# Kernel tuning notes

Measured on AMD Instinct MI355X. Metric: run time of the kernel, lower is better.

The kernel has to match this reference:

```python
import jax, jax.numpy as jnp
import numpy as np


def setup_inputs() -> dict:
    key = jax.random.key(0)
    ks = jax.random.split(key, 8)
    B, N, D, E, S = 8, 4096, 1024, 64, 2
    H = D
    T = E * S  # total slots = 128
    return {
        "x": jax.random.normal(ks[0], (B, N, D), jnp.float32),
        "phi_w": jax.random.normal(ks[1], (T, D), jnp.float32) * 0.02,
        "fc1_w": jax.random.normal(ks[2], (E, H, D), jnp.float32) * 0.02,
        "fc1_b": jax.random.normal(ks[3], (E, H), jnp.float32) * 0.02,
        "fc2_w": jax.random.normal(ks[4], (E, D, H), jnp.float32) * 0.02,
        "fc2_b": jax.random.normal(ks[5], (E, D), jnp.float32) * 0.02,
        "out_w": jax.random.normal(ks[6], (D, D), jnp.float32) * 0.02,
        "out_b": jax.random.normal(ks[7], (D,), jnp.float32) * 0.02,
    }


def reference(x, phi_w, fc1_w, fc1_b, fc2_w, fc2_b, out_w, out_b):
    B, N, D = x.shape
    E, H, _ = fc1_w.shape
    T = phi_w.shape[0]
    S = T // E
    # dispatch logits: (B, N, T)
    logits = jnp.einsum('bnd,td->bnt', x, phi_w)
    dispatch_w = jax.nn.softmax(logits, axis=1)  # softmax over tokens
    combine_w = jax.nn.softmax(logits, axis=2)   # softmax over slots
    # dispatch: compress tokens -> slots, (B, T, D) -> (B, E, S, D)
    slots = jnp.einsum('bnt,bnd->btd', dispatch_w, x).reshape(B, E, S, D)
    # per-expert tiny MLP (no weight duplication over B)
    h = jnp.einsum('besd,ehd->besh', slots, fc1_w) + fc1_b[None, :, None, :]
    h = jax.nn.gelu(h, approximate=True)  # tanh approximation, matches torch
    out = jnp.einsum('besh,edh->besd', h, fc2_w) + fc2_b[None, :, None, :]
    out = out.reshape(B, T, D)
    # combine: expand slots -> tokens
    combined = jnp.einsum('bnt,btd->bnd', combine_w, out)
    output = jnp.einsum('bnd,od->bno', combined, out_w) + out_b
    aux_loss = jnp.asarray(0.0, dtype=x.dtype)
    return output, aux_loss
```

## Files before the change

### kernel.cpp

```cpp
#include <hip/hip_runtime.h>
#include <math.h>

#define B_ 8
#define N_ 4096
#define D_ 1024
#define E_ 64
#define T_ 128

using bf16   = __bf16;
using bf16x4 = __attribute__((ext_vector_type(4))) __bf16;
using bf16x8 = __attribute__((ext_vector_type(8))) __bf16;
using f32x4  = __attribute__((ext_vector_type(4))) float;

#define MFMA16(a, b, c) __builtin_amdgcn_mfma_f32_16x16x32_bf16(a, b, c, 0, 0, 0)
#define LDK 72

__device__ __forceinline__ bf16x8 ldsfrag(const bf16* p) {
  const int lane = threadIdx.x & 63;
  return *(const bf16x8*)(p + (lane & 15) * LDK + (lane >> 4) * 8);
}

__global__ void k_convert(const float* __restrict__ phi, const float* __restrict__ ow,
                          bf16* __restrict__ phi_bf, bf16* __restrict__ ow_bf)
{
  if (blockIdx.x < 128) {
    int i = blockIdx.x * 256 + threadIdx.x;
    float4 v = ((const float4*)phi)[i];
    ((bf16x4*)phi_bf)[i] = (bf16x4){(bf16)v.x, (bf16)v.y, (bf16)v.z, (bf16)v.w};
  } else {
    int i = (blockIdx.x - 128) * 256 + threadIdx.x;
    float4 v = ((const float4*)ow)[i];
    ((bf16x4*)ow_bf)[i] = (bf16x4){(bf16)v.x, (bf16)v.y, (bf16)v.z, (bf16)v.w};
  }
}

__global__ __launch_bounds__(256) void k_logits(
    const float* __restrict__ X, const bf16* __restrict__ Phi,
    float* __restrict__ L, bf16* __restrict__ Xbf)
{
  __shared__ bf16 As[64][LDK];
  __shared__ bf16 Bs[128][LDK];
  const int m0 = blockIdx.x * 64;
  const int tid = threadIdx.x;
  const int wave = tid >> 6, lane = tid & 63;
  const int wm = (wave >> 1) * 32;
  const int wn = (wave & 1) * 64;

  f32x4 acc[2][4];
#pragma unroll
  for (int i = 0; i < 2; ++i)
#pragma unroll
    for (int j = 0; j < 4; ++j) acc[i][j] = (f32x4){0.f, 0.f, 0.f, 0.f};

  const int ar = tid >> 2, ac = (tid & 3) * 16;
  const int br = tid >> 1, bc = (tid & 1) * 32;

  for (int k0 = 0; k0 < 1024; k0 += 64) {
    const float* xp = X + (long)(m0 + ar) * 1024 + k0 + ac;
    float4 v0 = *(const float4*)(xp + 0);
    float4 v1 = *(const float4*)(xp + 4);
    float4 v2 = *(const float4*)(xp + 8);
    float4 v3 = *(const float4*)(xp + 12);
    bf16x8 p0 = {(bf16)v0.x, (bf16)v0.y, (bf16)v0.z, (bf16)v0.w,
                 (bf16)v1.x, (bf16)v1.y, (bf16)v1.z, (bf16)v1.w};
    bf16x8 p1 = {(bf16)v2.x, (bf16)v2.y, (bf16)v2.z, (bf16)v2.w,
                 (bf16)v3.x, (bf16)v3.y, (bf16)v3.z, (bf16)v3.w};
    *(bf16x8*)&As[ar][ac]     = p0;
    *(bf16x8*)&As[ar][ac + 8] = p1;
    bf16* xo = Xbf + (long)(m0 + ar) * 1024 + k0 + ac;
    *(bf16x8*)xo       = p0;
    *(bf16x8*)(xo + 8) = p1;

    const bf16* pp = Phi + (long)br * 1024 + k0 + bc;
    *(bf16x8*)&Bs[br][bc + 0]  = *(const bf16x8*)(pp + 0);
    *(bf16x8*)&Bs[br][bc + 8]  = *(const bf16x8*)(pp + 8);
    *(bf16x8*)&Bs[br][bc + 16] = *(const bf16x8*)(pp + 16);
    *(bf16x8*)&Bs[br][bc + 24] = *(const bf16x8*)(pp + 24);
    __syncthreads();
#pragma unroll
    for (int kk = 0; kk < 64; kk += 32) {
      bf16x8 a0 = ldsfrag(&As[wm][kk]);
      bf16x8 a1 = ldsfrag(&As[wm + 16][kk]);
#pragma unroll
      for (int n = 0; n < 4; ++n) {
        bf16x8 bb = ldsfrag(&Bs[wn + n * 16][kk]);
        acc[0][n] = MFMA16(a0, bb, acc[0][n]);
        acc[1][n] = MFMA16(a1, bb, acc[1][n]);
      }
    }
    __syncthreads();
  }
  const int cc = lane & 15, rr = (lane >> 4) * 4;
#pragma unroll
  for (int m = 0; m < 2; ++m)
#pragma unroll
    for (int n = 0; n < 4; ++n)
#pragma unroll
      for (int j = 0; j < 4; ++j)
        L[(long)(m0 + wm + m * 16 + rr + j) * 128 + wn + n * 16 + cc] = acc[m][n][j];
}

__global__ __launch_bounds__(256) void disp_partial(const float* __restrict__ L,
    float* __restrict__ redM, float* __restrict__ redS)
{
  const int chunk = blockIdx.x;
  const int b     = blockIdx.y;
  const int t    = threadIdx.x & 127;
  const int half = threadIdx.x >> 7;
  const float* Lb = L + (long)b * N_ * T_;
  float m = -1e30f, s = 0.f;
  for (int i = 0; i < 64; ++i) {
    int n = chunk * 128 + i * 2 + half;
    float v = Lb[(long)n * T_ + t];
    if (v > m) { s = s * expf(m - v) + 1.f; m = v; }
    else       { s += expf(v - m); }
  }
  __shared__ float sm[128], ss[128];
  if (half) { sm[t] = m; ss[t] = s; }
  __syncthreads();
  if (!half) {
    float m2 = sm[t], s2 = ss[t];
    float nm = fmaxf(m, m2);
    float ns = s * expf(m - nm) + s2 * expf(m2 - nm);
    redM[((long)b * 32 + chunk) * 128 + t] = nm;
    redS[((long)b * 32 + chunk) * 128 + t] = ns;
  }
}

__global__ void disp_final(const float* __restrict__ redM, const float* __restrict__ redS,
                           float* __restrict__ Mf, float* __restrict__ Zf)
{
  int idx = blockIdx.x * 256 + threadIdx.x;
  int b = idx >> 7, t = idx & 127;
  float m = -1e30f, s = 0.f;
  for (int c = 0; c < 32; ++c) {
    float mc = redM[((long)b * 32 + c) * 128 + t];
    float sc = redS[((long)b * 32 + c) * 128 + t];
    float nm = fmaxf(m, mc);
    s = s * expf(m - nm) + sc * expf(mc - nm);
    m = nm;
  }
  Mf[idx] = m;
  Zf[idx] = 1.f / s;
}

__global__ __launch_bounds__(256) void k_dwt(const float* __restrict__ L,
    const float* __restrict__ Mf, const float* __restrict__ Zf, bf16* __restrict__ DWT)
{
  __shared__ float S[64][132];
  const int b = blockIdx.y, n0 = blockIdx.x * 64;
  const int tid = threadIdx.x;
  const int r = tid >> 2;
  const int c0 = (tid & 3) * 32;
  const float* Lp = L + ((long)b * N_ + n0 + r) * T_ + c0;
#pragma unroll
  for (int i = 0; i < 32; i += 4) {
    float4 v = *(const float4*)(Lp + i);
    int tb = b * 128 + c0 + i;
    S[r][c0 + i + 0] = expf(v.x - Mf[tb + 0]) * Zf[tb + 0];
    S[r][c0 + i + 1] = expf(v.y - Mf[tb + 1]) * Zf[tb + 1];
    S[r][c0 + i + 2] = expf(v.z - Mf[tb + 2]) * Zf[tb + 2];
    S[r][c0 + i + 3] = expf(v.w - Mf[tb + 3]) * Zf[tb + 3];
  }
  __syncthreads();
  const int nc = (tid & 7) * 8;
  for (int ti = tid >> 3; ti < 128; ti += 32) {
    bf16x8 o;
#pragma unroll
    for (int j = 0; j < 8; ++j) o[j] = (bf16)S[nc + j][ti];
    *(bf16x8*)(DWT + ((long)b * 128 + ti) * 4096 + n0 + nc) = o;
  }
}

__global__ __launch_bounds__(256) void k_cw(const float* __restrict__ L, bf16* __restrict__ CW)
{
  const int row  = blockIdx.x * 4 + (threadIdx.x >> 6);
  const int lane = threadIdx.x & 63;
  const float* Lr = L + (long)row * T_;
  float v0 = Lr[lane], v1 = Lr[lane + 64];
  float m = fmaxf(v0, v1);
#pragma unroll
  for (int o = 32; o; o >>= 1) m = fmaxf(m, __shfl_xor(m, o));
  float e0 = expf(v0 - m), e1 = expf(v1 - m);
  float s = e0 + e1;
#pragma unroll
  for (int o = 32; o; o >>= 1) s += __shfl_xor(s, o);
  float inv = 1.f / s;
  CW[(long)row * T_ + lane]      = (bf16)(e0 * inv);
  CW[(long)row * T_ + lane + 64] = (bf16)(e1 * inv);
}

__global__ __launch_bounds__(256) void k_slots(
    const bf16* __restrict__ DWT, const bf16* __restrict__ Xbf, float* __restrict__ Part)
{
  __shared__ bf16 As[128][LDK];
  __shared__ bf16 Bs[128][LDK];
  const int b = blockIdx.z >> 3, chunk = blockIdx.z & 7;
  const int d0 = blockIdx.x * 128;
  const int tid = threadIdx.x, wave = tid >> 6, lane = tid & 63;
  const int wm = (wave >> 1) * 64, wn = (wave & 1) * 64;

  f32x4 acc[4][4];
#pragma unroll
  for (int i = 0; i < 4; ++i)
#pragma unroll
    for (int j = 0; j < 4; ++j) acc[i][j] = (f32x4){0.f, 0.f, 0.f, 0.f};

  const int at = tid >> 1, anc = (tid & 1) * 32;
  const int bn = tid >> 2, bdc = (tid & 3) * 32;
  const long dwt_b = (long)b * 128 * 4096;
  const long x_b   = (long)b * 4096 * 1024;

  for (int k0 = 0; k0 < 512; k0 += 64) {
    const int nbase = chunk * 512 + k0;
    const bf16* ap = DWT + dwt_b + (long)at * 4096 + nbase + anc;
    *(bf16x8*)&As[at][anc + 0]  = *(const bf16x8*)(ap + 0);
    *(bf16x8*)&As[at][anc + 8]  = *(const bf16x8*)(ap + 8);
    *(bf16x8*)&As[at][anc + 16] = *(const bf16x8*)(ap + 16);
    *(bf16x8*)&As[at][anc + 24] = *(const bf16x8*)(ap + 24);
    const bf16* xp = Xbf + x_b + (long)(nbase + bn) * 1024 + d0 + bdc;
    bf16x8 q0 = *(const bf16x8*)(xp + 0);
    bf16x8 q1 = *(const bf16x8*)(xp + 8);
    bf16x8 q2 = *(const bf16x8*)(xp + 16);
    bf16x8 q3 = *(const bf16x8*)(xp + 24);
#pragma unroll
    for (int i = 0; i < 8; ++i) {
      Bs[bdc + i][bn]      = q0[i];
      Bs[bdc + 8 + i][bn]  = q1[i];
      Bs[bdc + 16 + i][bn] = q2[i];
      Bs[bdc + 24 + i][bn] = q3[i];
    }
    __syncthreads();
#pragma unroll
    for (int kk = 0; kk < 64; kk += 32) {
      bf16x8 af[4], bfr[4];
#pragma unroll
      for (int m = 0; m < 4; ++m) af[m]  = ldsfrag(&As[wm + m * 16][kk]);
#pragma unroll
      for (int n = 0; n < 4; ++n) bfr[n] = ldsfrag(&Bs[wn + n * 16][kk]);
#pragma unroll
      for (int m = 0; m < 4; ++m)
#pragma unroll
        for (int n = 0; n < 4; ++n)
          acc[m][n] = MFMA16(af[m], bfr[n], acc[m][n]);
    }
    __syncthreads();
  }
  const int cc = lane & 15, rr = (lane >> 4) * 4;
  float* Cp = Part + (long)(chunk * 8 + b) * 128 * 1024;
#pragma unroll
  for (int m = 0; m < 4; ++m)
#pragma unroll
    for (int n = 0; n < 4; ++n)
#pragma unroll
      for (int j = 0; j < 4; ++j)
        Cp[(long)(wm + m * 16 + rr + j) * 1024 + d0 + wn + n * 16 + cc] = acc[m][n][j];
}

__global__ void k_reduce8(const float* __restrict__ P, bf16* __restrict__ O)
{
  long base = ((long)blockIdx.x * 256 + threadIdx.x) * 4;
  float4 s = *(const float4*)(P + base);
  for (int c = 1; c < 8; ++c) {
    float4 v = *(const float4*)(P + (long)c * 1048576 + base);
    s.x += v.x; s.y += v.y; s.z += v.z; s.w += v.w;
  }
  *(bf16x4*)(O + base) = (bf16x4){(bf16)s.x, (bf16)s.y, (bf16)s.z, (bf16)s.w};
}

template<int GELU, int INL>
__global__ __launch_bounds__(256) void k_expert(
    const bf16* __restrict__ Ab, const float* __restrict__ W,
    const float* __restrict__ bias, bf16* __restrict__ Out)
{
  __shared__ bf16 As[16][LDK];
  __shared__ bf16 Bs[64][LDK];
  const int e = blockIdx.y;
  const int h0 = blockIdx.x * 64;
  const int tid = threadIdx.x, wave = tid >> 6, lane = tid & 63;
  f32x4 acc = (f32x4){0.f, 0.f, 0.f, 0.f};

  const int hr = tid >> 2, kc = (tid & 3) * 16;

  for (int k0 = 0; k0 < 1024; k0 += 64) {
    if (tid < 128) {
      int r = tid >> 3, akc = (tid & 7) * 8;
      long row = (INL == 0) ? (long)((r >> 1) * 128 + e * 2 + (r & 1)) : (long)(e * 16 + r);
      *(bf16x8*)&As[r][akc] = *(const bf16x8*)(Ab + row * 1024 + k0 + akc);
    }
    const float* wp = W + ((long)e * 1024 + h0 + hr) * 1024 + k0 + kc;
    float4 w0 = *(const float4*)(wp + 0);
    float4 w1 = *(const float4*)(wp + 4);
    float4 w2 = *(const float4*)(wp + 8);
    float4 w3 = *(const float4*)(wp + 12);
    bf16x8 p0 = {(bf16)w0.x, (bf16)w0.y, (bf16)w0.z, (bf16)w0.w,
                 (bf16)w1.x, (bf16)w1.y, (bf16)w1.z, (bf16)w1.w};
    bf16x8 p1 = {(bf16)w2.x, (bf16)w2.y, (bf16)w2.z, (bf16)w2.w,
                 (bf16)w3.x, (bf16)w3.y, (bf16)w3.z, (bf16)w3.w};
    *(bf16x8*)&Bs[hr][kc]     = p0;
    *(bf16x8*)&Bs[hr][kc + 8] = p1;
    __syncthreads();
#pragma unroll
    for (int kk = 0; kk < 64; kk += 32) {
      bf16x8 a  = ldsfrag(&As[0][kk]);
      bf16x8 bb = ldsfrag(&Bs[wave * 16][kk]);
      acc = MFMA16(a, bb, acc);
    }
    __syncthreads();
  }
  const int cc = lane & 15, rr = (lane >> 4) * 4;
  const int h = h0 + wave * 16 + cc;
  const float bs = bias[e * 1024 + h];
#pragma unroll
  for (int j = 0; j < 4; ++j) {
    float v = acc[j] + bs;
    if (GELU) {
      float x3 = v * v * v;
      v = 0.5f * v * (1.f + tanhf(0.7978845608028654f * (v + 0.044715f * x3)));
    }
    int m = rr + j;
    long orow = (INL == 0) ? (long)(e * 16 + m) : (long)((m >> 1) * 128 + e * 2 + (m & 1));
    Out[orow * 1024 + h] = (bf16)v;
  }
}

__global__ __launch_bounds__(256) void k_proj(
    const bf16* __restrict__ OWbf, const bf16* __restrict__ OS, bf16* __restrict__ PT)
{
  __shared__ bf16 As[64][LDK];
  __shared__ bf16 Bs[64][LDK];
  const int o0 = blockIdx.y * 64, t0 = blockIdx.x * 64;
  const int tid = threadIdx.x, wave = tid >> 6, lane = tid & 63;
  const int wm = (wave >> 1) * 32, wn = (wave & 1) * 32;
  f32x4 acc[2][2];
#pragma unroll
  for (int i = 0; i < 2; ++i)
#pragma unroll
    for (int j = 0; j < 2; ++j) acc[i][j] = (f32x4){0.f, 0.f, 0.f, 0.f};

  const int r = tid >> 2, kc = (tid & 3) * 16;
  for (int k0 = 0; k0 < 1024; k0 += 64) {
    const bf16* apo = OWbf + (long)(o0 + r) * 1024 + k0 + kc;
    *(bf16x8*)&As[r][kc]     = *(const bf16x8*)(apo + 0);
    *(bf16x8*)&As[r][kc + 8] = *(const bf16x8*)(apo + 8);
    const bf16* bpo = OS + (long)(t0 + r) * 1024 + k0 + kc;
    *(bf16x8*)&Bs[r][kc]     = *(const bf16x8*)(bpo + 0);
    *(bf16x8*)&Bs[r][kc + 8] = *(const bf16x8*)(bpo + 8);
    __syncthreads();
#pragma unroll
    for (int kk = 0; kk < 64; kk += 32) {
      bf16x8 a0 = ldsfrag(&As[wm][kk]);
      bf16x8 a1 = ldsfrag(&As[wm + 16][kk]);
      bf16x8 b0 = ldsfrag(&Bs[wn][kk]);
      bf16x8 b1 = ldsfrag(&Bs[wn + 16][kk]);
      acc[0][0] = MFMA16(a0, b0, acc[0][0]);
      acc[0][1] = MFMA16(a0, b1, acc[0][1]);
      acc[1][0] = MFMA16(a1, b0, acc[1][0]);
      acc[1][1] = MFMA16(a1, b1, acc[1][1]);
    }
    __syncthreads();
  }
  const int cc = lane & 15, rr = (lane >> 4) * 4;
#pragma unroll
  for (int m = 0; m < 2; ++m)
#pragma unroll
    for (int n = 0; n < 2; ++n)
#pragma unroll
      for (int j = 0; j < 4; ++j)
        PT[(long)(o0 + wm + m * 16 + rr + j) * 1024 + t0 + wn + n * 16 + cc] =
            (bf16)acc[m][n][j];
}

__global__ __launch_bounds__(256) void k_combine(
    const bf16* __restrict__ CW, const bf16* __restrict__ PT,
    const float* __restrict__ ob, float* __restrict__ O)
{
  __shared__ bf16 As[128][LDK];
  __shared__ bf16 Bs[128][LDK];
  const int b = blockIdx.z, m0 = blockIdx.y * 128, o0 = blockIdx.x * 128;
  const int tid = threadIdx.x, wave = tid >> 6, lane = tid & 63;
  const int wm = (wave >> 1) * 64, wn = (wave & 1) * 64;

  f32x4 acc[4][4];
#pragma unroll
  for (int i = 0; i < 4; ++i)
#pragma unroll
    for (int j = 0; j < 4; ++j) acc[i][j] = (f32x4){0.f, 0.f, 0.f, 0.f};

  const int r = tid >> 1, tc = (tid & 1) * 32;
  for (int k0 = 0; k0 < 128; k0 += 64) {
    const bf16* ap = CW + ((long)b * N_ + m0 + r) * 128 + k0 + tc;
    *(bf16x8*)&As[r][tc + 0]  = *(const bf16x8*)(ap + 0);
    *(bf16x8*)&As[r][tc + 8]  = *(const bf16x8*)(ap + 8);
    *(bf16x8*)&As[r][tc + 16] = *(const bf16x8*)(ap + 16);
    *(bf16x8*)&As[r][tc + 24] = *(const bf16x8*)(ap + 24);
    const bf16* bp = PT + (long)(o0 + r) * 1024 + b * 128 + k0 + tc;
    *(bf16x8*)&Bs[r][tc + 0]  = *(const bf16x8*)(bp + 0);
    *(bf16x8*)&Bs[r][tc + 8]  = *(const bf16x8*)(bp + 8);
    *(bf16x8*)&Bs[r][tc + 16] = *(const bf16x8*)(bp + 16);
    *(bf16x8*)&Bs[r][tc + 24] = *(const bf16x8*)(bp + 24);
    __syncthreads();
#pragma unroll
    for (int kk = 0; kk < 64; kk += 32) {
      bf16x8 af[4], bfr[4];
#pragma unroll
      for (int m = 0; m < 4; ++m) af[m]  = ldsfrag(&As[wm + m * 16][kk]);
#pragma unroll
      for (int n = 0; n < 4; ++n) bfr[n] = ldsfrag(&Bs[wn + n * 16][kk]);
#pragma unroll
      for (int m = 0; m < 4; ++m)
#pragma unroll
        for (int n = 0; n < 4; ++n)
          acc[m][n] = MFMA16(af[m], bfr[n], acc[m][n]);
    }
    __syncthreads();
  }
  const int cc = lane & 15, rr = (lane >> 4) * 4;
#pragma unroll
  for (int n = 0; n < 4; ++n) {
    const int o = o0 + wn + n * 16 + cc;
    const float bv = ob[o];
#pragma unroll
    for (int m = 0; m < 4; ++m)
#pragma unroll
      for (int j = 0; j < 4; ++j)
        O[((long)b * N_ + m0 + wm + m * 16 + rr + j) * 1024 + o] = acc[m][n][j] + bv;
  }
}

__global__ void write_aux(float* __restrict__ out) { out[(long)B_ * N_ * D_] = 0.f; }

extern "C" void kernel_launch(void* const* d_in, const int* in_sizes, int n_in,
                              void* d_out, int out_size, void* d_ws, size_t ws_size,
                              hipStream_t stream)
{
  const float* x     = (const float*)d_in[0];
  const float* phi_w = (const float*)d_in[1];
  const float* fc1_w = (const float*)d_in[2];
  const float* fc1_b = (const float*)d_in[3];
  const float* fc2_w = (const float*)d_in[4];
  const float* fc2_b = (const float*)d_in[5];
  const float* out_w = (const float*)d_in[6];
  const float* out_b = (const float*)d_in[7];
  float* out = (float*)d_out;

  float* ws     = (float*)d_ws;
  float* logits = ws;
  float* redM   = logits + 4194304;
  float* redS   = redM + 32768;
  float* Mf     = redS + 32768;
  float* Zf     = Mf + 1024;
  bf16* DWT     = (bf16*)(Zf + 1024);
  bf16* CW      = DWT + 4194304;
  bf16* slots   = CW + 4194304;
  bf16* hbuf    = slots + 1048576;
  bf16* outs    = hbuf + 1048576;
  bf16* projT   = outs + 1048576;
  bf16* phi_bf  = projT + 1048576;
  bf16* outw_bf = phi_bf + 131072;

  bf16* Xbf   = (bf16*)d_out;
  float* Part = (float*)d_out + 16777216;

  k_convert<<<dim3(1152), 256, 0, stream>>>(phi_w, out_w, phi_bf, outw_bf);
  k_logits<<<dim3(512), 256, 0, stream>>>(x, phi_bf, logits, Xbf);
  disp_partial<<<dim3(32, 8), 256, 0, stream>>>(logits, redM, redS);
  disp_final<<<dim3(4), 256, 0, stream>>>(redM, redS, Mf, Zf);
  k_dwt<<<dim3(64, 8), 256, 0, stream>>>(logits, Mf, Zf, DWT);
  k_cw<<<dim3(8192), 256, 0, stream>>>(logits, CW);
  k_slots<<<dim3(8, 1, 64), 256, 0, stream>>>(DWT, Xbf, Part);
  k_reduce8<<<dim3(1024), 256, 0, stream>>>(Part, slots);
  k_expert<1, 0><<<dim3(16, 64), 256, 0, stream>>>(slots, fc1_w, fc1_b, hbuf);
  k_expert<0, 1><<<dim3(16, 64), 256, 0, stream>>>(hbuf, fc2_w, fc2_b, outs);
  k_proj<<<dim3(16, 16), 256, 0, stream>>>(outw_bf, outs, projT);
  k_combine<<<dim3(8, 32, 8), 256, 0, stream>>>(CW, projT, out_b, out);
  write_aux<<<1, 1, 0, stream>>>(out);
}
```

Before: 344.1 us.

## Fuse combine softmax and dispatch partial reductions into logits GEMM epilogue

The logits GEMM now stages its output tile in shared memory and computes the per-token combine softmax (writing CW) plus per-64-row online max/sum partials for the dispatch softmax. This removes the separate k_cw and disp_partial kernels and their re-reads of the logits buffer. disp_final now reduces twice as many chunks, k_dwt applies the exp/normalise during its transpose, and the aux-zero write moves into k_combine. The cost is extra epilogue work and a serial 64-row loop in the GEMM blocks that may lengthen their tail.

```diff
diff --git a/kernel.cpp b/kernel.cpp
--- a/kernel.cpp
+++ b/kernel.cpp
@@ -18,6 +18,11 @@
 __device__ __forceinline__ bf16x8 ldsfrag(const bf16* p) {
   const int lane = threadIdx.x & 63;
   return *(const bf16x8*)(p + (lane & 15) * LDK + (lane >> 4) * 8);
+}
+
+__device__ __forceinline__ bf16x8 cvt8(float4 a, float4 b) {
+  return (bf16x8){(bf16)a.x, (bf16)a.y, (bf16)a.z, (bf16)a.w,
+                  (bf16)b.x, (bf16)b.y, (bf16)b.z, (bf16)b.w};
 }
 
 __global__ void k_convert(const float* __restrict__ phi, const float* __restrict__ ow,
@@ -36,10 +41,14 @@
 
 __global__ __launch_bounds__(256) void k_logits(
     const float* __restrict__ X, const bf16* __restrict__ Phi,
-    float* __restrict__ L, bf16* __restrict__ Xbf)
-{
-  __shared__ bf16 As[64][LDK];
-  __shared__ bf16 Bs[128][LDK];
+    float* __restrict__ L, bf16* __restrict__ Xbf, bf16* __restrict__ CW,
+    float* __restrict__ redM, float* __restrict__ redS)
+{
+  __shared__ __align__(16) char smraw[34048];
+  bf16 (*As)[LDK] = (bf16(*)[LDK])smraw;
+  bf16 (*Bs)[LDK] = (bf16(*)[LDK])(smraw + 64 * LDK * 2);
+  float (*S)[133] = (float(*)[133])smraw;
+
   const int m0 = blockIdx.x * 64;
   const int tid = threadIdx.x;
   const int wave = tid >> 6, lane = tid & 63;
@@ -61,10 +70,8 @@
     float4 v1 = *(const float4*)(xp + 4);
     float4 v2 = *(const float4*)(xp + 8);
     float4 v3 = *(const float4*)(xp + 12);
-    bf16x8 p0 = {(bf16)v0.x, (bf16)v0.y, (bf16)v0.z, (bf16)v0.w,
-                 (bf16)v1.x, (bf16)v1.y, (bf16)v1.z, (bf16)v1.w};
-    bf16x8 p1 = {(bf16)v2.x, (bf16)v2.y, (bf16)v2.z, (bf16)v2.w,
-                 (bf16)v3.x, (bf16)v3.y, (bf16)v3.z, (bf16)v3.w};
+    bf16x8 p0 = cvt8(v0, v1);
+    bf16x8 p1 = cvt8(v2, v3);
     *(bf16x8*)&As[ar][ac]     = p0;
     *(bf16x8*)&As[ar][ac + 8] = p1;
     bf16* xo = Xbf + (long)(m0 + ar) * 1024 + k0 + ac;
@@ -96,34 +103,47 @@
 #pragma unroll
     for (int n = 0; n < 4; ++n)
 #pragma unroll
-      for (int j = 0; j < 4; ++j)
-        L[(long)(m0 + wm + m * 16 + rr + j) * 128 + wn + n * 16 + cc] = acc[m][n][j];
-}
-
-__global__ __launch_bounds__(256) void disp_partial(const float* __restrict__ L,
-    float* __restrict__ redM, float* __restrict__ redS)
-{
-  const int chunk = blockIdx.x;
-  const int b     = blockIdx.y;
-  const int t    = threadIdx.x & 127;
-  const int half = threadIdx.x >> 7;
-  const float* Lb = L + (long)b * N_ * T_;
-  float m = -1e30f, s = 0.f;
-  for (int i = 0; i < 64; ++i) {
-    int n = chunk * 128 + i * 2 + half;
-    float v = Lb[(long)n * T_ + t];
-    if (v > m) { s = s * expf(m - v) + 1.f; m = v; }
-    else       { s += expf(v - m); }
-  }
-  __shared__ float sm[128], ss[128];
-  if (half) { sm[t] = m; ss[t] = s; }
+      for (int j = 0; j < 4; ++j) {
+        const float val = acc[m][n][j];
+        L[(long)(m0 + wm + m * 16 + rr + j) * 128 + wn + n * 16 + cc] = val;
+        S[wm + m * 16 + rr + j][wn + n * 16 + cc] = val;
+      }
   __syncthreads();
-  if (!half) {
-    float m2 = sm[t], s2 = ss[t];
-    float nm = fmaxf(m, m2);
-    float ns = s * expf(m - nm) + s2 * expf(m2 - nm);
-    redM[((long)b * 32 + chunk) * 128 + t] = nm;
-    redS[((long)b * 32 + chunk) * 128 + t] = ns;
+
+  const int r = tid >> 2, q = tid & 3;
+  float v[32];
+#pragma unroll
+  for (int i = 0; i < 8; ++i)
+#pragma unroll
+    for (int j = 0; j < 4; ++j) v[i * 4 + j] = S[r][q * 4 + i * 16 + j];
+  float mx = -1e30f;
+#pragma unroll
+  for (int i = 0; i < 32; ++i) mx = fmaxf(mx, v[i]);
+  mx = fmaxf(mx, __shfl_xor(mx, 1));
+  mx = fmaxf(mx, __shfl_xor(mx, 2));
+  float sum = 0.f;
+#pragma unroll
+  for (int i = 0; i < 32; ++i) { v[i] = expf(v[i] - mx); sum += v[i]; }
+  sum += __shfl_xor(sum, 1);
+  sum += __shfl_xor(sum, 2);
+  const float inv = 1.f / sum;
+  bf16* cwr = CW + (long)(m0 + r) * 128 + q * 4;
+#pragma unroll
+  for (int i = 0; i < 8; ++i)
+    *(bf16x4*)(cwr + i * 16) = (bf16x4){(bf16)(v[i*4+0]*inv), (bf16)(v[i*4+1]*inv),
+                                        (bf16)(v[i*4+2]*inv), (bf16)(v[i*4+3]*inv)};
+
+  if (tid < 128) {
+    const int t = tid;
+    float m = -1e30f, s = 0.f;
+    for (int rj = 0; rj < 64; ++rj) {
+      float val = S[rj][t];
+      if (val > m) { s = s * expf(m - val) + 1.f; m = val; }
+      else         { s += expf(val - m); }
+    }
+    const long chunk = m0 >> 6;
+    redM[chunk * 128 + t] = m;
+    redS[chunk * 128 + t] = s;
   }
 }
 
@@ -133,9 +153,9 @@
   int idx = blockIdx.x * 256 + threadIdx.x;
   int b = idx >> 7, t = idx & 127;
   float m = -1e30f, s = 0.f;
-  for (int c = 0; c < 32; ++c) {
-    float mc = redM[((long)b * 32 + c) * 128 + t];
-    float sc = redS[((long)b * 32 + c) * 128 + t];
+  for (int c = 0; c < 64; ++c) {
+    float mc = redM[((long)b * 64 + c) * 128 + t];
+    float sc = redS[((long)b * 64 + c) * 128 + t];
     float nm = fmaxf(m, mc);
     s = s * expf(m - nm) + sc * expf(mc - nm);
     m = nm;
@@ -156,38 +176,20 @@
 #pragma unroll
   for (int i = 0; i < 32; i += 4) {
     float4 v = *(const float4*)(Lp + i);
-    int tb = b * 128 + c0 + i;
-    S[r][c0 + i + 0] = expf(v.x - Mf[tb + 0]) * Zf[tb + 0];
-    S[r][c0 + i + 1] = expf(v.y - Mf[tb + 1]) * Zf[tb + 1];
-    S[r][c0 + i + 2] = expf(v.z - Mf[tb + 2]) * Zf[tb + 2];
-    S[r][c0 + i + 3] = expf(v.w - Mf[tb + 3]) * Zf[tb + 3];
+    S[r][c0 + i + 0] = v.x;
+    S[r][c0 + i + 1] = v.y;
+    S[r][c0 + i + 2] = v.z;
+    S[r][c0 + i + 3] = v.w;
   }
   __syncthreads();
   const int nc = (tid & 7) * 8;
   for (int ti = tid >> 3; ti < 128; ti += 32) {
+    const float mf = Mf[b * 128 + ti], zf = Zf[b * 128 + ti];
     bf16x8 o;
 #pragma unroll
-    for (int j = 0; j < 8; ++j) o[j] = (bf16)S[nc + j][ti];
+    for (int j = 0; j < 8; ++j) o[j] = (bf16)(expf(S[nc + j][ti] - mf) * zf);
     *(bf16x8*)(DWT + ((long)b * 128 + ti) * 4096 + n0 + nc) = o;
   }
-}
-
-__global__ __launch_bounds__(256) void k_cw(const float* __restrict__ L, bf16* __restrict__ CW)
-{
-  const int row  = blockIdx.x * 4 + (threadIdx.x >> 6);
-  const int lane = threadIdx.x & 63;
-  const float* Lr = L + (long)row * T_;
-  float v0 = Lr[lane], v1 = Lr[lane + 64];
-  float m = fmaxf(v0, v1);
-#pragma unroll
-  for (int o = 32; o; o >>= 1) m = fmaxf(m, __shfl_xor(m, o));
-  float e0 = expf(v0 - m), e1 = expf(v1 - m);
-  float s = e0 + e1;
-#pragma unroll
-  for (int o = 32; o; o >>= 1) s += __shfl_xor(s, o);
-  float inv = 1.f / s;
-  CW[(long)row * T_ + lane]      = (bf16)(e0 * inv);
-  CW[(long)row * T_ + lane + 64] = (bf16)(e1 * inv);
 }
 
 __global__ __launch_bounds__(256) void k_slots(
@@ -247,7 +249,7 @@
     __syncthreads();
   }
   const int cc = lane & 15, rr = (lane >> 4) * 4;
-  float* Cp = Part + (long)(chunk * 8 + b) * 128 * 1024;
+  float* Cp = Part + ((long)chunk * 8 + b) * 128 * 1024;
 #pragma unroll
   for (int m = 0; m < 4; ++m)
 #pragma unroll
@@ -293,19 +295,15 @@
     float4 w1 = *(const float4*)(wp + 4);
     float4 w2 = *(const float4*)(wp + 8);
     float4 w3 = *(const float4*)(wp + 12);
-    bf16x8 p0 = {(bf16)w0.x, (bf16)w0.y, (bf16)w0.z, (bf16)w0.w,
-                 (bf16)w1.x, (bf16)w1.y, (bf16)w1.z, (bf16)w1.w};
-    bf16x8 p1 = {(bf16)w2.x, (bf16)w2.y, (bf16)w2.z, (bf16)w2.w,
-                 (bf16)w3.x, (bf16)w3.y, (bf16)w3.z, (bf16)w3.w};
-    *(bf16x8*)&Bs[hr][kc]     = p0;
-    *(bf16x8*)&Bs[hr][kc + 8] = p1;
-    __syncthreads();
-#pragma unroll
-    for (int kk = 0; kk < 64; kk += 32) {
-      bf16x8 a  = ldsfrag(&As[0][kk]);
-      bf16x8 bb = ldsfrag(&Bs[wave * 16][kk]);
-      acc = MFMA16(a, bb, acc);
-    }
+    *(bf16x8*)&Bs[hr][kc]     = cvt8(w0, w1);
+    *(bf16x8*)&Bs[hr][kc + 8] = cvt8(w2, w3);
+    __syncthreads();
+    bf16x8 a0 = ldsfrag(&As[0][0]);
+    bf16x8 b0 = ldsfrag(&Bs[wave * 16][0]);
+    acc = MFMA16(a0, b0, acc);
+    a0 = ldsfrag(&As[0][32]);
+    b0 = ldsfrag(&Bs[wave * 16][32]);
+    acc = MFMA16(a0, b0, acc);
     __syncthreads();
   }
   const int cc = lane & 15, rr = (lane >> 4) * 4;
@@ -380,6 +378,9 @@
   const int b = blockIdx.z, m0 = blockIdx.y * 128, o0 = blockIdx.x * 128;
   const int tid = threadIdx.x, wave = tid >> 6, lane = tid & 63;
   const int wm = (wave >> 1) * 64, wn = (wave & 1) * 64;
+
+  if (blockIdx.x == 0 && blockIdx.y == 0 && blockIdx.z == 0 && tid == 0)
+    O[(long)B_ * N_ * D_] = 0.f;
 
   f32x4 acc[4][4];
 #pragma unroll
@@ -428,8 +429,6 @@
   }
 }
 
-__global__ void write_aux(float* __restrict__ out) { out[(long)B_ * N_ * D_] = 0.f; }
-
 extern "C" void kernel_launch(void* const* d_in, const int* in_sizes, int n_in,
                               void* d_out, int out_size, void* d_ws, size_t ws_size,
                               hipStream_t stream)
@@ -447,8 +446,8 @@
   float* ws     = (float*)d_ws;
   float* logits = ws;
   float* redM   = logits + 4194304;
-  float* redS   = redM + 32768;
-  float* Mf     = redS + 32768;
+  float* redS   = redM + 65536;
+  float* Mf     = redS + 65536;
   float* Zf     = Mf + 1024;
   bf16* DWT     = (bf16*)(Zf + 1024);
   bf16* CW      = DWT + 4194304;
@@ -463,16 +462,13 @@
   float* Part = (float*)d_out + 16777216;
 
   k_convert<<<dim3(1152), 256, 0, stream>>>(phi_w, out_w, phi_bf, outw_bf);
-  k_logits<<<dim3(512), 256, 0, stream>>>(x, phi_bf, logits, Xbf);
-  disp_partial<<<dim3(32, 8), 256, 0, stream>>>(logits, redM, redS);
+  k_logits<<<dim3(512), 256, 0, stream>>>(x, phi_bf, logits, Xbf, CW, redM, redS);
   disp_final<<<dim3(4), 256, 0, stream>>>(redM, redS, Mf, Zf);
   k_dwt<<<dim3(64, 8), 256, 0, stream>>>(logits, Mf, Zf, DWT);
-  k_cw<<<dim3(8192), 256, 0, stream>>>(logits, CW);
   k_slots<<<dim3(8, 1, 64), 256, 0, stream>>>(DWT, Xbf, Part);
   k_reduce8<<<dim3(1024), 256, 0, stream>>>(Part, slots);
   k_expert<1, 0><<<dim3(16, 64), 256, 0, stream>>>(slots, fc1_w, fc1_b, hbuf);
   k_expert<0, 1><<<dim3(16, 64), 256, 0, stream>>>(hbuf, fc2_w, fc2_b, outs);
   k_proj<<<dim3(16, 16), 256, 0, stream>>>(outw_bf, outs, projT);
   k_combine<<<dim3(8, 32, 8), 256, 0, stream>>>(CW, projT, out_b, out);
-  write_aux<<<1, 1, 0, stream>>>(out);
-}
+}
```

Result: faster. 325.6 us (-5.4%).
